# Kernel tuning notes

Hardware: AMD Instinct MI355X
Metric: run time of the kernel (lower is better)

The kernel has to match this reference:

```python
import jax, jax.numpy as jnp
import numpy as np

# ---- config (from cfg / InstantNGP defaults) ----
W_IMG, H_IMG = 1024, 1024            # uv_reso_w, uv_reso_h
N_LEVELS = 16                        # standard InstantNGP level count
BASE_RES = 16
FINEST_RES = 1024                    # cfg['finest_level']
F_FEAT = 2                           # features per level
LOG2_T = 19                          # cfg['log2_hashmap_size']
T = 1 << LOG2_T
HIDDEN = 64
PRIMES = np.array([1, 2654435761], dtype=np.uint32)  # 2D spatial-hash primes


def setup_inputs() -> dict:
    key = jax.random.key(0)
    ks = jax.random.split(key, 5)
    d_in = N_LEVELS * F_FEAT
    tables = jax.random.uniform(ks[0], (N_LEVELS, T, F_FEAT), jnp.float32, -1e-4, 1e-4)
    W1 = jax.random.normal(ks[1], (d_in, HIDDEN), jnp.float32) / np.sqrt(d_in)
    b1 = jnp.zeros((HIDDEN,), jnp.float32)
    W2 = jax.random.normal(ks[2], (HIDDEN, HIDDEN), jnp.float32) / np.sqrt(HIDDEN)
    b2 = jnp.zeros((HIDDEN,), jnp.float32)
    W3 = jax.random.normal(ks[3], (HIDDEN, 3), jnp.float32) / np.sqrt(HIDDEN)
    b3 = jnp.zeros((3,), jnp.float32)
    return {"tables": tables, "W1": W1, "b1": b1, "W2": W2, "b2": b2, "W3": W3, "b3": b3}


def _uv_coords():
    # replicate torch.meshgrid(arange(W), arange(H), indexing='xy') -> (H, W)
    xx, yy = jnp.meshgrid(jnp.arange(W_IMG), jnp.arange(H_IMG), indexing='xy')
    x = xx.ravel().astype(jnp.float32) / W_IMG
    y = yy.ravel().astype(jnp.float32) / H_IMG
    return jnp.stack([x, y], axis=1)  # [N, 2]


def _hash_encode(coord, tables):
    # coord: [N,2] in [0,1); tables: [L,T,F]
    growth = np.exp((np.log(FINEST_RES) - np.log(BASE_RES)) / (N_LEVELS - 1))
    res = np.floor(BASE_RES * growth ** np.arange(N_LEVELS)).astype(np.float32)  # [L]
    scaled = coord[None, :, :] * res[:, None, None]          # [L,N,2]
    c0f = jnp.floor(scaled)
    frac = scaled - c0f                                       # [L,N,2]
    c0 = c0f.astype(jnp.uint32)
    corners = jnp.array([[0, 0], [1, 0], [0, 1], [1, 1]], dtype=jnp.uint32)  # [4,2]
    cc = c0[:, :, None, :] + corners[None, None]              # [L,N,4,2]
    idx = (cc[..., 0] * jnp.uint32(PRIMES[0])) ^ (cc[..., 1] * jnp.uint32(PRIMES[1]))
    idx = (idx & jnp.uint32(T - 1)).astype(jnp.int32)         # [L,N,4]
    feats = jax.vmap(lambda tab, i: tab[i])(tables, idx)      # [L,N,4,F] scattered gather
    cf = corners.astype(jnp.float32)                          # [4,2]
    # bilinear weights: prod over dims of (frac if corner bit else 1-frac)
    w = jnp.prod(cf[None, None] * frac[:, :, None, :] +
                 (1.0 - cf[None, None]) * (1.0 - frac[:, :, None, :]), axis=-1)  # [L,N,4]
    feat = jnp.einsum('lnc,lncf->lnf', w, feats)              # [L,N,F]
    return jnp.transpose(feat, (1, 0, 2)).reshape(-1, N_LEVELS * F_FEAT)  # [N, L*F]


def reference(tables, W1, b1, W2, b2, W3, b3):
    coord = _uv_coords()                                      # [N,2]
    enc = _hash_encode(coord, tables)                         # [N,32]
    h = jax.nn.relu(enc @ W1 + b1)
    h = jax.nn.relu(h @ W2 + b2)
    out = h @ W3 + b3                                         # [N,3]
    img = out.reshape(H_IMG, W_IMG, 3).transpose(2, 0, 1)     # [3,H,W]
    return jax.nn.sigmoid(img)[None, ...]                     # [1,3,H,W]
```

## Files before the change

### kernel.cpp

```cpp
#include <hip/hip_runtime.h>
#include <math.h>

#define NLEV   16
#define TSIZE  524288
#define TMASK  524287
#define NPIX   (1024*1024)

typedef __attribute__((ext_vector_type(8))) short s8v;
typedef __attribute__((ext_vector_type(4))) float f4v;

struct ResArr { float r[NLEV]; };
union Frag { unsigned int u[4]; s8v v; };

__device__ __forceinline__ unsigned short bf16_rn(float x) {
    unsigned int u = __builtin_bit_cast(unsigned int, x);
    u += 0x7fffu + ((u >> 16) & 1u);
    return (unsigned short)(u >> 16);
}
__device__ __forceinline__ unsigned int pk_bf16(float lo, float hi) {
    return __builtin_amdgcn_perm(__builtin_bit_cast(unsigned int, hi),
                                 __builtin_bit_cast(unsigned int, lo),
                                 0x07060302u);
}

__global__ __launch_bounds__(256) void prep_kernel(
    const float* __restrict__ W1, const float* __restrict__ W2,
    const float* __restrict__ W3, float* __restrict__ ws, ResArr res)
{
    const int t = threadIdx.x;
    if (t < NLEV) ws[t] = res.r[t];
    unsigned short* w1t = (unsigned short*)(ws + 16);
    unsigned short* w2t = w1t + 64 * 32;
    unsigned short* w3t = w2t + 64 * 64;
    for (int i = t; i < 64 * 32; i += 256) {
        int n = i >> 5, k = i & 31;
        w1t[i] = bf16_rn(W1[k * 64 + n]);
    }
    for (int i = t; i < 64 * 64; i += 256) {
        int n2 = i >> 6, kp = i & 63;
        int klog = (kp & 32) | ((kp & 4) << 2) | ((kp & 24) >> 1) | (kp & 3);
        w2t[i] = bf16_rn(W2[klog * 64 + n2]);
    }
    for (int i = t; i < 16 * 64; i += 256) {
        int row = i >> 6, kp = i & 63;
        int klog = (kp & 32) | ((kp & 4) << 2) | ((kp & 24) >> 1) | (kp & 3);
        int ch = row & 3;
        w3t[i] = (ch < 3) ? bf16_rn(W3[klog * 3 + ch]) : (unsigned short)0;
    }
}

__global__ __launch_bounds__(256) void ngp_mfma_kernel(
    const float* __restrict__ tables,
    const float* __restrict__ b1, const float* __restrict__ b2,
    const float* __restrict__ b3,
    const float* __restrict__ ws, float* __restrict__ out)
{
    const int tid  = threadIdx.x;
    const int lane = tid & 63;
    const int wv   = tid >> 6;
    const int c15  = lane & 15;
    const int g    = lane >> 4;
    const int xb   = blockIdx.x * 16;
    const int yb   = blockIdx.y * 16;

    const float4 rv = *(const float4*)(ws + g * 4);
    const float rr[4] = { rv.x, rv.y, rv.z, rv.w };
    const float xs = (float)(xb + c15) * (1.0f / 1024.0f);
    float yf[4];
    #pragma unroll
    for (int pt = 0; pt < 4; ++pt)
        yf[pt] = (float)(yb + wv * 4 + pt) * (1.0f / 1024.0f);

    const float2* __restrict__ tabg = (const float2*)tables + (size_t)(g * 4) * TSIZE;

    float2 fb[2][4][4];
    float  fxb[2];
    float  fyb[2][4];
    Frag   bfrag[4];

#define NGP_ISSUE(J, B) do {                                                  \
    const float r_   = rr[J];                                                 \
    const float sx_  = xs * r_;                                               \
    const float fx0_ = floorf(sx_);                                           \
    fxb[B] = sx_ - fx0_;                                                      \
    const unsigned int cx_  = (unsigned int)fx0_;                             \
    const unsigned int cx1_ = cx_ + 1u;                                       \
    const float2* __restrict__ tab_ = tabg + (size_t)(J) * TSIZE;             \
    _Pragma("unroll")                                                         \
    for (int pt_ = 0; pt_ < 4; ++pt_) {                                       \
        const float sy_  = yf[pt_] * r_;                                      \
        const float fy0_ = floorf(sy_);                                       \
        fyb[B][pt_] = sy_ - fy0_;                                             \
        const unsigned int cy_  = (unsigned int)fy0_;                         \
        const unsigned int hy0_ = cy_ * 2654435761u;                          \
        const unsigned int hy1_ = hy0_ + 2654435761u;                         \
        fb[B][pt_][0] = tab_[(cx_  ^ hy0_) & TMASK];                          \
        fb[B][pt_][1] = tab_[(cx1_ ^ hy0_) & TMASK];                          \
        fb[B][pt_][2] = tab_[(cx_  ^ hy1_) & TMASK];                          \
        fb[B][pt_][3] = tab_[(cx1_ ^ hy1_) & TMASK];                          \
    }                                                                         \
    asm volatile("" ::: "memory");                                            \
} while (0)

#define NGP_CONSUME(J, B) do {                                                \
    const float fx_ = fxb[B];                                                 \
    _Pragma("unroll")                                                         \
    for (int pt_ = 0; pt_ < 4; ++pt_) {                                       \
        const float fy_  = fyb[B][pt_];                                       \
        const float w00_ = (1.0f - fx_) * (1.0f - fy_);                       \
        const float w10_ = fx_          * (1.0f - fy_);                       \
        const float w01_ = (1.0f - fx_) * fy_;                                \
        const float w11_ = fx_          * fy_;                                \
        const float e0_ = w00_ * fb[B][pt_][0].x + w10_ * fb[B][pt_][1].x     \
                        + w01_ * fb[B][pt_][2].x + w11_ * fb[B][pt_][3].x;    \
        const float e1_ = w00_ * fb[B][pt_][0].y + w10_ * fb[B][pt_][1].y     \
                        + w01_ * fb[B][pt_][2].y + w11_ * fb[B][pt_][3].y;    \
        bfrag[pt_].u[J] = pk_bf16(e0_, e1_);                                  \
    }                                                                         \
} while (0)

    const unsigned short* __restrict__ w1t = (const unsigned short*)(ws + 16);
    const unsigned short* __restrict__ w2t = w1t + 64 * 32;
    const unsigned short* __restrict__ w3t = w2t + 64 * 64;
    Frag afr[4];

    NGP_ISSUE(0, 0);
    NGP_ISSUE(1, 1);
    NGP_CONSUME(0, 0);
    NGP_ISSUE(2, 0);
    NGP_CONSUME(1, 1);
    NGP_ISSUE(3, 1);
    #pragma unroll
    for (int mt = 0; mt < 4; ++mt)
        afr[mt].v = *(const s8v*)(w1t + (mt * 16 + c15) * 32 + g * 8);
    asm volatile("" ::: "memory");
    NGP_CONSUME(2, 0);
    NGP_CONSUME(3, 1);

#undef NGP_ISSUE
#undef NGP_CONSUME

    unsigned int hp[4][4][2];
    #pragma unroll
    for (int mt = 0; mt < 4; ++mt) {
        const float4 bb = *(const float4*)(b1 + mt * 16 + g * 4);
        #pragma unroll
        for (int pt = 0; pt < 4; ++pt) {
            f4v acc = (f4v){0.f, 0.f, 0.f, 0.f};
            acc = __builtin_amdgcn_mfma_f32_16x16x32_bf16(
                afr[mt].v, bfrag[pt].v, acc, 0, 0, 0);
            const float v0 = fmaxf(acc[0] + bb.x, 0.0f);
            const float v1 = fmaxf(acc[1] + bb.y, 0.0f);
            const float v2 = fmaxf(acc[2] + bb.z, 0.0f);
            const float v3 = fmaxf(acc[3] + bb.w, 0.0f);
            hp[mt][pt][0] = pk_bf16(v0, v1);
            hp[mt][pt][1] = pk_bf16(v2, v3);
        }
    }

    unsigned int hq[4][4][2];
    #pragma unroll
    for (int mt = 0; mt < 4; ++mt) {
        const float4 bb2 = *(const float4*)(b2 + mt * 16 + g * 4);
        f4v acc[4];
        #pragma unroll
        for (int pt = 0; pt < 4; ++pt) acc[pt] = (f4v){0.f, 0.f, 0.f, 0.f};
        #pragma unroll
        for (int st = 0; st < 2; ++st) {
            Frag a2, bf2[4];
            a2.v = *(const s8v*)(w2t + (mt * 16 + c15) * 64 + st * 32 + g * 8);
            #pragma unroll
            for (int pt = 0; pt < 4; ++pt) {
                bf2[pt].u[0] = hp[2 * st + 0][pt][0];
                bf2[pt].u[1] = hp[2 * st + 0][pt][1];
                bf2[pt].u[2] = hp[2 * st + 1][pt][0];
                bf2[pt].u[3] = hp[2 * st + 1][pt][1];
            }
            #pragma unroll
            for (int pt = 0; pt < 4; ++pt)
                acc[pt] = __builtin_amdgcn_mfma_f32_16x16x32_bf16(
                    a2.v, bf2[pt].v, acc[pt], 0, 0, 0);
        }
        #pragma unroll
        for (int pt = 0; pt < 4; ++pt) {
            const float v0 = fmaxf(acc[pt][0] + bb2.x, 0.0f);
            const float v1 = fmaxf(acc[pt][1] + bb2.y, 0.0f);
            const float v2 = fmaxf(acc[pt][2] + bb2.z, 0.0f);
            const float v3 = fmaxf(acc[pt][3] + bb2.w, 0.0f);
            hq[mt][pt][0] = pk_bf16(v0, v1);
            hq[mt][pt][1] = pk_bf16(v2, v3);
        }
    }

    f4v acc3[4];
    #pragma unroll
    for (int pt = 0; pt < 4; ++pt) acc3[pt] = (f4v){0.f, 0.f, 0.f, 0.f};
    #pragma unroll
    for (int st = 0; st < 2; ++st) {
        Frag a3, bf3[4];
        a3.v = *(const s8v*)(w3t + c15 * 64 + st * 32 + g * 8);
        #pragma unroll
        for (int pt = 0; pt < 4; ++pt) {
            bf3[pt].u[0] = hq[2 * st + 0][pt][0];
            bf3[pt].u[1] = hq[2 * st + 0][pt][1];
            bf3[pt].u[2] = hq[2 * st + 1][pt][0];
            bf3[pt].u[3] = hq[2 * st + 1][pt][1];
        }
        #pragma unroll
        for (int pt = 0; pt < 4; ++pt)
            acc3[pt] = __builtin_amdgcn_mfma_f32_16x16x32_bf16(
                a3.v, bf3[pt].v, acc3[pt], 0, 0, 0);
    }

    float ov[3];
    #pragma unroll
    for (int c = 0; c < 3; ++c) {
        float v = acc3[0][c];
        v = (g == 1) ? acc3[1][c] : v;
        v = (g == 2) ? acc3[2][c] : v;
        v = (g == 3) ? acc3[3][c] : v;
        ov[c] = v + b3[c];
    }
    const int pix = ((yb + wv * 4 + g) << 10) + xb + c15;
    out[0 * NPIX + pix] = 1.0f / (1.0f + __expf(-ov[0]));
    out[1 * NPIX + pix] = 1.0f / (1.0f + __expf(-ov[1]));
    out[2 * NPIX + pix] = 1.0f / (1.0f + __expf(-ov[2]));
}

extern "C" void kernel_launch(void* const* d_in, const int* in_sizes, int n_in,
                              void* d_out, int out_size, void* d_ws, size_t ws_size,
                              hipStream_t stream) {
    const float* tables = (const float*)d_in[0];
    const float* W1     = (const float*)d_in[1];
    const float* b1     = (const float*)d_in[2];
    const float* W2     = (const float*)d_in[3];
    const float* b2     = (const float*)d_in[4];
    const float* W3     = (const float*)d_in[5];
    const float* b3     = (const float*)d_in[6];
    float* out          = (float*)d_out;
    float* ws           = (float*)d_ws;

    ResArr res;
    const double growth = exp((log(1024.0) - log(16.0)) / 15.0);
    for (int l = 0; l < NLEV; ++l)
        res.r[l] = (float)floor(16.0 * pow(growth, (double)l));

    hipLaunchKernelGGL(prep_kernel, dim3(1), dim3(256), 0, stream, W1, W2, W3, ws, res);
    hipLaunchKernelGGL(ngp_mfma_kernel, dim3(64, 64), dim3(256), 0, stream,
                       tables, b1, b2, b3, ws, out);
}
```

Before: 67.93 us.

## Split fused kernel into hash-encode and MLP kernels via workspace buffer

Splits the fused encoder+MLP kernel into two launches. The encoder kernel does the hash gathers with a two-stage software pipeline and a forced occupancy of 4 waves per EU, then writes bf16 encodings (64 MB) to workspace. A separate MLP kernel reads them back and runs the MFMA layers. The point is to let the gather-bound and compute-bound phases each run at their own best occupancy and register budget, at the cost of a large extra global write and read and one more launch. If the workspace is too small, it falls back to the fused kernel.

```diff
diff --git a/kernel.cpp b/kernel.cpp
--- a/kernel.cpp
+++ b/kernel.cpp
@@ -5,6 +5,7 @@
 #define TSIZE  524288
 #define TMASK  524287
 #define NPIX   (1024*1024)
+#define ENC_OFF_BYTES 32768
 
 typedef __attribute__((ext_vector_type(8))) short s8v;
 typedef __attribute__((ext_vector_type(4))) float f4v;
@@ -49,7 +50,207 @@
     }
 }
 
-__global__ __launch_bounds__(256) void ngp_mfma_kernel(
+__global__ __launch_bounds__(256) __attribute__((amdgpu_waves_per_eu(4, 4)))
+void ngp_enc_kernel(const float* __restrict__ tables,
+                    const float* __restrict__ ws,
+                    unsigned int* __restrict__ enc)
+{
+    const int tid  = threadIdx.x;
+    const int lane = tid & 63;
+    const int wv   = tid >> 6;
+    const int c15  = lane & 15;
+    const int g    = lane >> 4;
+    const int xb   = blockIdx.x * 16;
+    const int yb   = blockIdx.y * 16;
+
+    const float4 rv = *(const float4*)(ws + g * 4);
+    const float rr[4] = { rv.x, rv.y, rv.z, rv.w };
+    const float xs = (float)(xb + c15) * (1.0f / 1024.0f);
+    float yf[4];
+    #pragma unroll
+    for (int pt = 0; pt < 4; ++pt)
+        yf[pt] = (float)(yb + wv * 4 + pt) * (1.0f / 1024.0f);
+
+    const float2* __restrict__ tabg = (const float2*)tables + (size_t)(g * 4) * TSIZE;
+
+    float2 fb[2][4][4];
+    float  fxb[2];
+    float  fyb[2][4];
+    Frag   bfrag[4];
+
+#define ENC_ISSUE(J, B) do {                                                  \
+    const float r_   = rr[J];                                                 \
+    const float sx_  = xs * r_;                                               \
+    const float fx0_ = floorf(sx_);                                           \
+    fxb[B] = sx_ - fx0_;                                                      \
+    const unsigned int cx_  = (unsigned int)fx0_;                             \
+    const unsigned int cx1_ = cx_ + 1u;                                       \
+    const float2* __restrict__ tab_ = tabg + (size_t)(J) * TSIZE;             \
+    _Pragma("unroll")                                                         \
+    for (int pt_ = 0; pt_ < 4; ++pt_) {                                       \
+        const float sy_  = yf[pt_] * r_;                                      \
+        const float fy0_ = floorf(sy_);                                       \
+        fyb[B][pt_] = sy_ - fy0_;                                             \
+        const unsigned int cy_  = (unsigned int)fy0_;                         \
+        const unsigned int hy0_ = cy_ * 2654435761u;                          \
+        const unsigned int hy1_ = hy0_ + 2654435761u;                         \
+        fb[B][pt_][0] = tab_[(cx_  ^ hy0_) & TMASK];                          \
+        fb[B][pt_][1] = tab_[(cx1_ ^ hy0_) & TMASK];                          \
+        fb[B][pt_][2] = tab_[(cx_  ^ hy1_) & TMASK];                          \
+        fb[B][pt_][3] = tab_[(cx1_ ^ hy1_) & TMASK];                          \
+    }                                                                         \
+    asm volatile("" ::: "memory");                                            \
+} while (0)
+
+#define ENC_CONSUME(J, B) do {                                                \
+    const float fx_ = fxb[B];                                                 \
+    _Pragma("unroll")                                                         \
+    for (int pt_ = 0; pt_ < 4; ++pt_) {                                       \
+        const float fy_  = fyb[B][pt_];                                       \
+        const float w00_ = (1.0f - fx_) * (1.0f - fy_);                       \
+        const float w10_ = fx_          * (1.0f - fy_);                       \
+        const float w01_ = (1.0f - fx_) * fy_;                                \
+        const float w11_ = fx_          * fy_;                                \
+        const float e0_ = w00_ * fb[B][pt_][0].x + w10_ * fb[B][pt_][1].x     \
+                        + w01_ * fb[B][pt_][2].x + w11_ * fb[B][pt_][3].x;    \
+        const float e1_ = w00_ * fb[B][pt_][0].y + w10_ * fb[B][pt_][1].y     \
+                        + w01_ * fb[B][pt_][2].y + w11_ * fb[B][pt_][3].y;    \
+        bfrag[pt_].u[J] = pk_bf16(e0_, e1_);                                  \
+    }                                                                         \
+} while (0)
+
+    ENC_ISSUE(0, 0);
+    ENC_ISSUE(1, 1);
+    ENC_CONSUME(0, 0);
+    ENC_ISSUE(2, 0);
+    ENC_CONSUME(1, 1);
+    ENC_ISSUE(3, 1);
+    ENC_CONSUME(2, 0);
+    ENC_CONSUME(3, 1);
+
+#undef ENC_ISSUE
+#undef ENC_CONSUME
+
+    #pragma unroll
+    for (int pt = 0; pt < 4; ++pt) {
+        const int row = ((yb + wv * 4 + pt) << 10) + xb + c15;
+        *(uint4*)(enc + (size_t)row * 16 + g * 4) = *(const uint4*)&bfrag[pt];
+    }
+}
+
+__global__ __launch_bounds__(256) void ngp_mlp_kernel(
+    const unsigned int* __restrict__ enc,
+    const float* __restrict__ b1, const float* __restrict__ b2,
+    const float* __restrict__ b3,
+    const float* __restrict__ ws, float* __restrict__ out)
+{
+    const int tid  = threadIdx.x;
+    const int lane = tid & 63;
+    const int wv   = tid >> 6;
+    const int c15  = lane & 15;
+    const int g    = lane >> 4;
+    const int base = (blockIdx.x * 4 + wv) * 64;
+
+    Frag bfrag[4];
+    #pragma unroll
+    for (int pt = 0; pt < 4; ++pt)
+        *(uint4*)&bfrag[pt] =
+            *(const uint4*)(enc + (size_t)(base + pt * 16 + c15) * 16 + g * 4);
+
+    const unsigned short* __restrict__ w1t = (const unsigned short*)(ws + 16);
+    const unsigned short* __restrict__ w2t = w1t + 64 * 32;
+    const unsigned short* __restrict__ w3t = w2t + 64 * 64;
+
+    unsigned int hp[4][4][2];
+    #pragma unroll
+    for (int mt = 0; mt < 4; ++mt) {
+        Frag afr;
+        afr.v = *(const s8v*)(w1t + (mt * 16 + c15) * 32 + g * 8);
+        const float4 bb = *(const float4*)(b1 + mt * 16 + g * 4);
+        #pragma unroll
+        for (int pt = 0; pt < 4; ++pt) {
+            f4v acc = (f4v){0.f, 0.f, 0.f, 0.f};
+            acc = __builtin_amdgcn_mfma_f32_16x16x32_bf16(
+                afr.v, bfrag[pt].v, acc, 0, 0, 0);
+            const float v0 = fmaxf(acc[0] + bb.x, 0.0f);
+            const float v1 = fmaxf(acc[1] + bb.y, 0.0f);
+            const float v2 = fmaxf(acc[2] + bb.z, 0.0f);
+            const float v3 = fmaxf(acc[3] + bb.w, 0.0f);
+            hp[mt][pt][0] = pk_bf16(v0, v1);
+            hp[mt][pt][1] = pk_bf16(v2, v3);
+        }
+    }
+
+    unsigned int hq[4][4][2];
+    #pragma unroll
+    for (int mt = 0; mt < 4; ++mt) {
+        const float4 bb2 = *(const float4*)(b2 + mt * 16 + g * 4);
+        f4v acc[4];
+        #pragma unroll
+        for (int pt = 0; pt < 4; ++pt) acc[pt] = (f4v){0.f, 0.f, 0.f, 0.f};
+        #pragma unroll
+        for (int st = 0; st < 2; ++st) {
+            Frag a2, bf2[4];
+            a2.v = *(const s8v*)(w2t + (mt * 16 + c15) * 64 + st * 32 + g * 8);
+            #pragma unroll
+            for (int pt = 0; pt < 4; ++pt) {
+                bf2[pt].u[0] = hp[2 * st + 0][pt][0];
+                bf2[pt].u[1] = hp[2 * st + 0][pt][1];
+                bf2[pt].u[2] = hp[2 * st + 1][pt][0];
+                bf2[pt].u[3] = hp[2 * st + 1][pt][1];
+            }
+            #pragma unroll
+            for (int pt = 0; pt < 4; ++pt)
+                acc[pt] = __builtin_amdgcn_mfma_f32_16x16x32_bf16(
+                    a2.v, bf2[pt].v, acc[pt], 0, 0, 0);
+        }
+        #pragma unroll
+        for (int pt = 0; pt < 4; ++pt) {
+            const float v0 = fmaxf(acc[pt][0] + bb2.x, 0.0f);
+            const float v1 = fmaxf(acc[pt][1] + bb2.y, 0.0f);
+            const float v2 = fmaxf(acc[pt][2] + bb2.z, 0.0f);
+            const float v3 = fmaxf(acc[pt][3] + bb2.w, 0.0f);
+            hq[mt][pt][0] = pk_bf16(v0, v1);
+            hq[mt][pt][1] = pk_bf16(v2, v3);
+        }
+    }
+
+    f4v acc3[4];
+    #pragma unroll
+    for (int pt = 0; pt < 4; ++pt) acc3[pt] = (f4v){0.f, 0.f, 0.f, 0.f};
+    #pragma unroll
+    for (int st = 0; st < 2; ++st) {
+        Frag a3, bf3[4];
+        a3.v = *(const s8v*)(w3t + c15 * 64 + st * 32 + g * 8);
+        #pragma unroll
+        for (int pt = 0; pt < 4; ++pt) {
+            bf3[pt].u[0] = hq[2 * st + 0][pt][0];
+            bf3[pt].u[1] = hq[2 * st + 0][pt][1];
+            bf3[pt].u[2] = hq[2 * st + 1][pt][0];
+            bf3[pt].u[3] = hq[2 * st + 1][pt][1];
+        }
+        #pragma unroll
+        for (int pt = 0; pt < 4; ++pt)
+            acc3[pt] = __builtin_amdgcn_mfma_f32_16x16x32_bf16(
+                a3.v, bf3[pt].v, acc3[pt], 0, 0, 0);
+    }
+
+    float ov[3];
+    #pragma unroll
+    for (int c = 0; c < 3; ++c) {
+        float v = acc3[0][c];
+        v = (g == 1) ? acc3[1][c] : v;
+        v = (g == 2) ? acc3[2][c] : v;
+        v = (g == 3) ? acc3[3][c] : v;
+        ov[c] = v + b3[c];
+    }
+    const int pix = base + g * 16 + c15;
+    out[0 * NPIX + pix] = 1.0f / (1.0f + __expf(-ov[0]));
+    out[1 * NPIX + pix] = 1.0f / (1.0f + __expf(-ov[1]));
+    out[2 * NPIX + pix] = 1.0f / (1.0f + __expf(-ov[2]));
+}
+
+__global__ __launch_bounds__(256) void ngp_fused_kernel(
     const float* __restrict__ tables,
     const float* __restrict__ b1, const float* __restrict__ b2,
     const float* __restrict__ b3,
@@ -246,6 +447,16 @@
         res.r[l] = (float)floor(16.0 * pow(growth, (double)l));
 
     hipLaunchKernelGGL(prep_kernel, dim3(1), dim3(256), 0, stream, W1, W2, W3, ws, res);
-    hipLaunchKernelGGL(ngp_mfma_kernel, dim3(64, 64), dim3(256), 0, stream,
-                       tables, b1, b2, b3, ws, out);
-}
+
+    const size_t need = (size_t)ENC_OFF_BYTES + (size_t)NPIX * 64;
+    if (ws_size >= need) {
+        unsigned int* enc = (unsigned int*)((char*)d_ws + ENC_OFF_BYTES);
+        hipLaunchKernelGGL(ngp_enc_kernel, dim3(64, 64), dim3(256), 0, stream,
+                           tables, ws, enc);
+        hipLaunchKernelGGL(ngp_mlp_kernel, dim3(4096), dim3(256), 0, stream,
+                           enc, b1, b2, b3, ws, out);
+    } else {
+        hipLaunchKernelGGL(ngp_fused_kernel, dim3(64, 64), dim3(256), 0, stream,
+                           tables, b1, b2, b3, ws, out);
+    }
+}
```

Result: slower. 78.24 us (+15.2%).

## Stage coarse-level hash corners in LDS per tile, gather fine levels directly

Applied to the files above, without the earlier changes.

For the 12 coarsest levels, each 16x16 pixel tile touches only a small grid of hash corners (3x3 up to 7x7, 221 total). The block now loads those corners once into shared memory cooperatively, and lanes for levels 0-11 interpolate from LDS. Only the 4 finest levels still do scattered global gathers. This cuts redundant global gather traffic and latency, at the cost of a block-wide barrier, divergent per-group code paths, and losing the previous software-pipelined issue/consume ordering.

```diff
diff --git a/kernel.cpp b/kernel.cpp
--- a/kernel.cpp
+++ b/kernel.cpp
@@ -49,12 +49,16 @@
     }
 }
 
-__global__ __launch_bounds__(256) void ngp_mfma_kernel(
+#define NCORN 221
+
+__global__ __launch_bounds__(256) void ngp_fused_kernel(
     const float* __restrict__ tables,
     const float* __restrict__ b1, const float* __restrict__ b2,
     const float* __restrict__ b3,
     const float* __restrict__ ws, float* __restrict__ out)
 {
+    __shared__ float2 ldsc[NCORN];
+
     const int tid  = threadIdx.x;
     const int lane = tid & 63;
     const int wv   = tid >> 6;
@@ -63,6 +67,32 @@
     const int xb   = blockIdx.x * 16;
     const int yb   = blockIdx.y * 16;
 
+    constexpr int WCL[12]  = {3,3,3,3,3,3,4,4,5,5,6,7};
+    constexpr int OFFL[12] = {0,9,18,27,36,45,54,70,86,111,136,172};
+
+    const float xbf = (float)xb * (1.0f / 1024.0f);
+    const float ybf = (float)yb * (1.0f / 1024.0f);
+
+    if (tid < NCORN) {
+        #pragma unroll
+        for (int l = 0; l < 12; ++l) {
+            const int sz = WCL[l] * WCL[l];
+            if (tid >= OFFL[l] && tid < OFFL[l] + sz) {
+                const int local = tid - OFFL[l];
+                const int jj = local / WCL[l];
+                const int ii = local - jj * WCL[l];
+                const float r = ws[l];
+                const int cx0 = (int)floorf(xbf * r);
+                const int cy0 = (int)floorf(ybf * r);
+                const unsigned int idx =
+                    (((unsigned int)(cx0 + ii)) ^
+                     ((unsigned int)(cy0 + jj) * 2654435761u)) & TMASK;
+                ldsc[tid] = ((const float2*)tables)[(size_t)l * TSIZE + idx];
+            }
+        }
+    }
+    __syncthreads();
+
     const float4 rv = *(const float4*)(ws + g * 4);
     const float rr[4] = { rv.x, rv.y, rv.z, rv.w };
     const float xs = (float)(xb + c15) * (1.0f / 1024.0f);
@@ -71,84 +101,88 @@
     for (int pt = 0; pt < 4; ++pt)
         yf[pt] = (float)(yb + wv * 4 + pt) * (1.0f / 1024.0f);
 
-    const float2* __restrict__ tabg = (const float2*)tables + (size_t)(g * 4) * TSIZE;
-
-    float2 fb[2][4][4];
-    float  fxb[2];
-    float  fyb[2][4];
-    Frag   bfrag[4];
-
-#define NGP_ISSUE(J, B) do {                                                  \
-    const float r_   = rr[J];                                                 \
-    const float sx_  = xs * r_;                                               \
-    const float fx0_ = floorf(sx_);                                           \
-    fxb[B] = sx_ - fx0_;                                                      \
-    const unsigned int cx_  = (unsigned int)fx0_;                             \
-    const unsigned int cx1_ = cx_ + 1u;                                       \
-    const float2* __restrict__ tab_ = tabg + (size_t)(J) * TSIZE;             \
-    _Pragma("unroll")                                                         \
-    for (int pt_ = 0; pt_ < 4; ++pt_) {                                       \
-        const float sy_  = yf[pt_] * r_;                                      \
-        const float fy0_ = floorf(sy_);                                       \
-        fyb[B][pt_] = sy_ - fy0_;                                             \
-        const unsigned int cy_  = (unsigned int)fy0_;                         \
-        const unsigned int hy0_ = cy_ * 2654435761u;                          \
-        const unsigned int hy1_ = hy0_ + 2654435761u;                         \
-        fb[B][pt_][0] = tab_[(cx_  ^ hy0_) & TMASK];                          \
-        fb[B][pt_][1] = tab_[(cx1_ ^ hy0_) & TMASK];                          \
-        fb[B][pt_][2] = tab_[(cx_  ^ hy1_) & TMASK];                          \
-        fb[B][pt_][3] = tab_[(cx1_ ^ hy1_) & TMASK];                          \
-    }                                                                         \
-    asm volatile("" ::: "memory");                                            \
-} while (0)
-
-#define NGP_CONSUME(J, B) do {                                                \
-    const float fx_ = fxb[B];                                                 \
-    _Pragma("unroll")                                                         \
-    for (int pt_ = 0; pt_ < 4; ++pt_) {                                       \
-        const float fy_  = fyb[B][pt_];                                       \
-        const float w00_ = (1.0f - fx_) * (1.0f - fy_);                       \
-        const float w10_ = fx_          * (1.0f - fy_);                       \
-        const float w01_ = (1.0f - fx_) * fy_;                                \
-        const float w11_ = fx_          * fy_;                                \
-        const float e0_ = w00_ * fb[B][pt_][0].x + w10_ * fb[B][pt_][1].x     \
-                        + w01_ * fb[B][pt_][2].x + w11_ * fb[B][pt_][3].x;    \
-        const float e1_ = w00_ * fb[B][pt_][0].y + w10_ * fb[B][pt_][1].y     \
-                        + w01_ * fb[B][pt_][2].y + w11_ * fb[B][pt_][3].y;    \
-        bfrag[pt_].u[J] = pk_bf16(e0_, e1_);                                  \
-    }                                                                         \
-} while (0)
+    Frag bfrag[4];
+
+    if (g < 3) {
+        #pragma unroll
+        for (int j = 0; j < 4; ++j) {
+            const int lWc  = (g == 0) ? WCL[j]  : (g == 1) ? WCL[4 + j]  : WCL[8 + j];
+            const int lOff = (g == 0) ? OFFL[j] : (g == 1) ? OFFL[4 + j] : OFFL[8 + j];
+            const float r   = rr[j];
+            const float sx  = xs * r;
+            const float fx0 = floorf(sx);
+            const float fx  = sx - fx0;
+            const int ii    = (int)fx0 - (int)floorf(xbf * r);
+            const int cy0i  = (int)floorf(ybf * r);
+            #pragma unroll
+            for (int pt = 0; pt < 4; ++pt) {
+                const float sy  = yf[pt] * r;
+                const float fy0 = floorf(sy);
+                const float fy  = sy - fy0;
+                const int jj    = (int)fy0 - cy0i;
+                const int base  = lOff + jj * lWc + ii;
+                const float2 c00 = ldsc[base];
+                const float2 c10 = ldsc[base + 1];
+                const float2 c01 = ldsc[base + lWc];
+                const float2 c11 = ldsc[base + lWc + 1];
+                const float w00 = (1.0f - fx) * (1.0f - fy);
+                const float w10 = fx          * (1.0f - fy);
+                const float w01 = (1.0f - fx) * fy;
+                const float w11 = fx          * fy;
+                bfrag[pt].u[j] = pk_bf16(
+                    w00 * c00.x + w10 * c10.x + w01 * c01.x + w11 * c11.x,
+                    w00 * c00.y + w10 * c10.y + w01 * c01.y + w11 * c11.y);
+            }
+        }
+    } else {
+        #pragma unroll
+        for (int j = 0; j < 4; ++j) {
+            const float r   = rr[j];
+            const float sx  = xs * r;
+            const float fx0 = floorf(sx);
+            const float fx  = sx - fx0;
+            const unsigned int cx  = (unsigned int)fx0;
+            const unsigned int cx1 = cx + 1u;
+            const float2* __restrict__ tab =
+                (const float2*)tables + (size_t)(12 + j) * TSIZE;
+            #pragma unroll
+            for (int pt = 0; pt < 4; ++pt) {
+                const float sy  = yf[pt] * r;
+                const float fy0 = floorf(sy);
+                const float fy  = sy - fy0;
+                const unsigned int cy  = (unsigned int)fy0;
+                const unsigned int hy0 = cy * 2654435761u;
+                const unsigned int hy1 = hy0 + 2654435761u;
+                const float2 f00 = tab[(cx  ^ hy0) & TMASK];
+                const float2 f10 = tab[(cx1 ^ hy0) & TMASK];
+                const float2 f01 = tab[(cx  ^ hy1) & TMASK];
+                const float2 f11 = tab[(cx1 ^ hy1) & TMASK];
+                const float w00 = (1.0f - fx) * (1.0f - fy);
+                const float w10 = fx          * (1.0f - fy);
+                const float w01 = (1.0f - fx) * fy;
+                const float w11 = fx          * fy;
+                bfrag[pt].u[j] = pk_bf16(
+                    w00 * f00.x + w10 * f10.x + w01 * f01.x + w11 * f11.x,
+                    w00 * f00.y + w10 * f10.y + w01 * f01.y + w11 * f11.y);
+            }
+        }
+    }
 
     const unsigned short* __restrict__ w1t = (const unsigned short*)(ws + 16);
     const unsigned short* __restrict__ w2t = w1t + 64 * 32;
     const unsigned short* __restrict__ w3t = w2t + 64 * 64;
-    Frag afr[4];
-
-    NGP_ISSUE(0, 0);
-    NGP_ISSUE(1, 1);
-    NGP_CONSUME(0, 0);
-    NGP_ISSUE(2, 0);
-    NGP_CONSUME(1, 1);
-    NGP_ISSUE(3, 1);
-    #pragma unroll
-    for (int mt = 0; mt < 4; ++mt)
-        afr[mt].v = *(const s8v*)(w1t + (mt * 16 + c15) * 32 + g * 8);
-    asm volatile("" ::: "memory");
-    NGP_CONSUME(2, 0);
-    NGP_CONSUME(3, 1);
-
-#undef NGP_ISSUE
-#undef NGP_CONSUME
 
     unsigned int hp[4][4][2];
     #pragma unroll
     for (int mt = 0; mt < 4; ++mt) {
+        Frag afr;
+        afr.v = *(const s8v*)(w1t + (mt * 16 + c15) * 32 + g * 8);
         const float4 bb = *(const float4*)(b1 + mt * 16 + g * 4);
         #pragma unroll
         for (int pt = 0; pt < 4; ++pt) {
             f4v acc = (f4v){0.f, 0.f, 0.f, 0.f};
             acc = __builtin_amdgcn_mfma_f32_16x16x32_bf16(
-                afr[mt].v, bfrag[pt].v, acc, 0, 0, 0);
+                afr.v, bfrag[pt].v, acc, 0, 0, 0);
             const float v0 = fmaxf(acc[0] + bb.x, 0.0f);
             const float v1 = fmaxf(acc[1] + bb.y, 0.0f);
             const float v2 = fmaxf(acc[2] + bb.z, 0.0f);
@@ -246,6 +280,6 @@
         res.r[l] = (float)floor(16.0 * pow(growth, (double)l));
 
     hipLaunchKernelGGL(prep_kernel, dim3(1), dim3(256), 0, stream, W1, W2, W3, ws, res);
-    hipLaunchKernelGGL(ngp_mfma_kernel, dim3(64, 64), dim3(256), 0, stream,
+    hipLaunchKernelGGL(ngp_fused_kernel, dim3(64, 64), dim3(256), 0, stream,
                        tables, b1, b2, b3, ws, out);
 }
```

Result: slower. 77.29 us (+13.8%).
